# Kernel tuning notes

Hardware: AMD Instinct MI355X
Metric: run time of the kernel (lower is better)

Reference implementation:

```python
import jax, jax.numpy as jnp
import numpy as np

D_MODEL = 1024
D_INNER = 2048
D_STATE = 16
D_CONV = 4
DT_RANK = 128  # ceil(d_inner/16)
B, L = 4, 2048


def setup_inputs() -> dict:
    key = jax.random.key(0)
    ks = jax.random.split(key, 12)
    s = 0.02
    return {
        "x": jax.random.normal(ks[0], (B, L, D_MODEL), jnp.float32),
        "in_proj_w": jax.random.normal(ks[1], (2 * D_INNER, D_MODEL), jnp.float32) * s,
        "in_proj_b": jax.random.normal(ks[2], (2 * D_INNER,), jnp.float32) * s,
        "conv_w": jax.random.normal(ks[3], (D_INNER, 1, D_CONV), jnp.float32) * s,
        "conv_b": jax.random.normal(ks[4], (D_INNER,), jnp.float32) * s,
        "x_proj_w": jax.random.normal(ks[5], (DT_RANK + 2 * D_STATE, D_INNER), jnp.float32) * s,
        "dt_proj_w": jax.random.normal(ks[6], (D_INNER, DT_RANK), jnp.float32) * s,
        "dt_proj_b": jax.random.normal(ks[7], (D_INNER,), jnp.float32) * s,
        "A_log": jnp.log(jnp.tile(jnp.arange(1, D_STATE + 1, dtype=jnp.float32)[None, :], (D_INNER, 1))),
        "D": jnp.ones((D_INNER,), jnp.float32),
        "out_proj_w": jax.random.normal(ks[8], (D_MODEL, D_INNER), jnp.float32) * s,
        "out_proj_b": jax.random.normal(ks[9], (D_MODEL,), jnp.float32) * s,
    }


def _selective_scan(u, delta, A, B_ssm, C, Dp):
    # u, delta: [b, l, d]; B_ssm, C: [b, l, n]; A: [d, n]; Dp: [d]
    def step(h, inp):
        dlt, Bt, Ct, ut = inp  # [b,d],[b,n],[b,n],[b,d]
        dA = jnp.exp(dlt[..., None] * A)               # [b,d,n]
        dBu = dlt[..., None] * Bt[:, None, :] * ut[..., None]
        h = dA * h + dBu
        y = jnp.einsum('bdn,bn->bd', h, Ct)
        return h, y

    h0 = jnp.zeros((u.shape[0], A.shape[0], A.shape[1]), u.dtype)
    xs = (jnp.swapaxes(delta, 0, 1), jnp.swapaxes(B_ssm, 0, 1),
          jnp.swapaxes(C, 0, 1), jnp.swapaxes(u, 0, 1))
    _, ys = jax.lax.scan(step, h0, xs)                 # [l,b,d]
    return jnp.swapaxes(ys, 0, 1) + u * Dp             # [b,l,d]


def reference(x, in_proj_w, in_proj_b, conv_w, conv_b, x_proj_w,
              dt_proj_w, dt_proj_b, A_log, D, out_proj_w, out_proj_b):
    xr = x @ in_proj_w.T + in_proj_b                   # [b,l,2d]
    xc, res = jnp.split(xr, 2, axis=-1)
    # depthwise conv1d, torch padding='same' with k=4 -> pad (1, 2)
    xcl = jnp.swapaxes(xc, 1, 2)                       # [b,d,l]
    xcl = jax.lax.conv_general_dilated(
        xcl, conv_w, window_strides=(1,), padding=[(1, 2)],
        feature_group_count=D_INNER,
        dimension_numbers=('NCH', 'OIH', 'NCH')) + conv_b[None, :, None]
    xc = jnp.swapaxes(xcl, 1, 2)                       # [b,l,d]
    x_dbl = xc @ x_proj_w.T                            # [b,l,dt_rank+2n]
    d_dt, B_ssm, C = jnp.split(x_dbl, [DT_RANK, DT_RANK + D_STATE], axis=-1)
    delta = jax.nn.softplus(d_dt @ dt_proj_w.T + dt_proj_b)
    A = -jnp.exp(A_log)
    y = _selective_scan(xc, delta, A, B_ssm, C, D)     # [b,l,d]
    y = y * jax.nn.silu(res)
    return y @ out_proj_w.T + out_proj_b
```

## Files before the change

kernel.cpp:

```cpp
#include <hip/hip_runtime.h>
#include <hip/hip_bf16.h>
#include <hip/hip_fp16.h>


typedef _Float16 f16;
typedef __attribute__((ext_vector_type(4))) float f32x4;
typedef __attribute__((ext_vector_type(4))) _Float16 f16x4;
typedef __attribute__((ext_vector_type(8))) _Float16 f16x8;

#define AS1C(p) ((const __attribute__((address_space(1))) void*)(p))
#define AS3(p)  ((__attribute__((address_space(3))) void*)(p))

#define D_MODEL 1024
#define D_INNER 2048
#define LSEQ    2048
#define NB      4
#define NCH     32
#define CLEN    64
#define LOG2E   1.44269504f

__global__ void cvt_f32_to_f16(const float* __restrict__ in, f16* __restrict__ out, int n4) {
  int i = blockIdx.x * blockDim.x + threadIdx.x;
  if (i >= n4) return;
  f32x4 v = *(const f32x4*)(in + (size_t)i * 4);
  f16x4 o;
  o[0] = (f16)v[0]; o[1] = (f16)v[1]; o[2] = (f16)v[2]; o[3] = (f16)v[3];
  *(f16x4*)(out + (size_t)i * 4) = o;
}

__global__ void cvt_pad_xproj(const float* __restrict__ in, f16* __restrict__ out) {
  int i = blockIdx.x * blockDim.x + threadIdx.x;
  int idx = i << 2;
  int row = idx >> 11;
  f16x4 o;
  if (row < 160) {
    f32x4 v = *(const f32x4*)(in + idx);
    o[0] = (f16)v[0]; o[1] = (f16)v[1]; o[2] = (f16)v[2]; o[3] = (f16)v[3];
  } else {
    o[0] = (f16)0.f; o[1] = (f16)0.f; o[2] = (f16)0.f; o[3] = (f16)0.f;
  }
  *(f16x4*)(out + idx) = o;
}

template<int EPI, bool XSW>
__global__ __launch_bounds__(256) void gemm_f16(
    const f16* __restrict__ A, int lda,
    const f16* __restrict__ Bw, int K,
    const float* __restrict__ bias,
    void* __restrict__ O0, void* __restrict__ O1,
    int NV, int ldo, int gx)
{
  __shared__ f16 lA[128 * 32];
  __shared__ f16 lB[128 * 32];
  const int tid  = threadIdx.x;
  const int lane = tid & 63;
  const int wid  = tid >> 6;
  const int wr = wid >> 1, wc = wid & 1;

  int tn_i, tm_i;
  {
    const int bid = blockIdx.x;
    if constexpr (XSW) {
      const int nxs = gx >> 3;
      const int xcd = bid & 7;
      const int j   = bid >> 3;
      tn_i = xcd * nxs + j % nxs;
      tm_i = j / nxs;
    } else {
      tn_i = bid % gx;
      tm_i = bid / gx;
    }
  }
  const int tm = tm_i * 128, tn = tn_i * 128;

  f32x4 acc[4][4] = {};

  const int i4 = lane >> 2;
  const int k8 = (lane & 3) << 3;
  const int ca = wid << 1;
  const f16* Abase = A  + (size_t)(tm + ca * 16 + i4) * lda + k8;
  const f16* Bbase = Bw + (size_t)(tn + ca * 16 + i4) * K   + k8;

  const int nKT = K >> 5;
  for (int kt = 0; kt < nKT; ++kt) {
    const int ko = kt << 5;
    __syncthreads();
    __builtin_amdgcn_global_load_lds(AS1C(Abase + ko),                    AS3(lA + ca * 512),       16, 0, 0);
    __builtin_amdgcn_global_load_lds(AS1C(Abase + (size_t)16 * lda + ko), AS3(lA + ca * 512 + 512), 16, 0, 0);
    __builtin_amdgcn_global_load_lds(AS1C(Bbase + ko),                    AS3(lB + ca * 512),       16, 0, 0);
    __builtin_amdgcn_global_load_lds(AS1C(Bbase + (size_t)16 * K + ko),   AS3(lB + ca * 512 + 512), 16, 0, 0);
    __syncthreads();

    const int ro = lane & 15;
    const int kf = (lane >> 4) << 3;
    f16x8 af[4], bf[4];
#pragma unroll
    for (int mi = 0; mi < 4; ++mi)
      af[mi] = *(const f16x8*)(lA + (wr * 64 + mi * 16 + ro) * 32 + kf);
#pragma unroll
    for (int nj = 0; nj < 4; ++nj)
      bf[nj] = *(const f16x8*)(lB + (wc * 64 + nj * 16 + ro) * 32 + kf);
#pragma unroll
    for (int mi = 0; mi < 4; ++mi)
#pragma unroll
      for (int nj = 0; nj < 4; ++nj)
        acc[mi][nj] = __builtin_amdgcn_mfma_f32_16x16x32_f16(af[mi], bf[nj], acc[mi][nj], 0, 0, 0);
  }

#pragma unroll
  for (int mi = 0; mi < 4; ++mi) {
    const int rb = tm + wr * 64 + mi * 16 + ((lane >> 4) << 2);
#pragma unroll
    for (int nj = 0; nj < 4; ++nj) {
      const int gn = tn + wc * 64 + nj * 16 + (lane & 15);
      if (gn >= NV) continue;
      float bv = 0.f;
      if constexpr (EPI != 1) bv = bias[gn];
#pragma unroll
      for (int j = 0; j < 4; ++j) {
        const float v = acc[mi][nj][j] + bv;
        const size_t row = (size_t)(rb + j);
        if constexpr (EPI == 0) {
          if (gn < 2048) ((f16*)O0)[row * 2048 + gn] = (f16)v;
          else           ((f16*)O1)[row * 2048 + (gn - 2048)] = (f16)v;
        } else if constexpr (EPI == 1) {
          ((f16*)O0)[row * (size_t)ldo + gn] = (f16)v;
        } else if constexpr (EPI == 2) {
          const float sp = (v > 20.f) ? v : log1pf(__expf(v));
          ((f16*)O0)[row * (size_t)ldo + gn] = (f16)sp;
        } else {
          ((float*)O0)[row * (size_t)ldo + gn] = v;
        }
      }
    }
  }
}

__global__ __launch_bounds__(256) void conv1d_kernel(
    const f16* __restrict__ xin, const float* __restrict__ w,
    const float* __restrict__ cb, f16* __restrict__ xout)
{
  const int d0  = threadIdx.x << 3;
  const int bid = blockIdx.x;
  const int b   = bid >> 8;
  const int l0  = (bid & 255) << 3;
  float wv[4][8];
#pragma unroll
  for (int q = 0; q < 8; ++q) {
    f32x4 t = *(const f32x4*)(w + (size_t)(d0 + q) * 4);
    wv[0][q] = t[0]; wv[1][q] = t[1]; wv[2][q] = t[2]; wv[3][q] = t[3];
  }
  float bv[8];
  *(f32x4*)bv       = *(const f32x4*)(cb + d0);
  *(f32x4*)(bv + 4) = *(const f32x4*)(cb + d0 + 4);
  const size_t base = (size_t)b * LSEQ * D_INNER;
  for (int lt = l0; lt < l0 + 8; ++lt) {
    float acc[8];
#pragma unroll
    for (int q = 0; q < 8; ++q) acc[q] = bv[q];
#pragma unroll
    for (int j = 0; j < 4; ++j) {
      const int li = lt + j - 1;
      if (li < 0 || li >= LSEQ) continue;
      f16x8 v = *(const f16x8*)(xin + base + (size_t)li * D_INNER + d0);
#pragma unroll
      for (int q = 0; q < 8; ++q) acc[q] += wv[j][q] * (float)v[q];
    }
    f16x8 o;
#pragma unroll
    for (int q = 0; q < 8; ++q) o[q] = (f16)acc[q];
    *(f16x8*)(xout + base + (size_t)lt * D_INNER + d0) = o;
  }
}


__global__ __launch_bounds__(256) void scan_pass1(
    const f16* __restrict__ delta, const f16* __restrict__ u,
    const f16* __restrict__ xdbl, const float* __restrict__ A_log,
    float* __restrict__ chunkS, float* __restrict__ chunkH)
{
  const int tid = threadIdx.x;
  const int d = blockIdx.x * 256 + tid;
  const int c = blockIdx.y;
  const int b = blockIdx.z;
  __shared__ float bl[CLEN][16];
  {
    const int t = tid >> 2, q = tid & 3;
    if (q < 2) {
      f16x8 v = *(const f16x8*)(xdbl + ((size_t)(b * LSEQ + c * CLEN + t)) * 160 + 128 + q * 8);
      float* dst = &bl[t][q * 8];
#pragma unroll
      for (int e = 0; e < 8; ++e) dst[e] = (float)v[e];
    }
  }
  __syncthreads();

  float An2[16], h[16];
  const float* alp = A_log + (size_t)d * 16;
#pragma unroll
  for (int n = 0; n < 16; ++n) { An2[n] = -__expf(alp[n]) * LOG2E; h[n] = 0.f; }

  float dsum = 0.f;
  const size_t base = ((size_t)(b * LSEQ + c * CLEN)) * D_INNER + d;
  float dl[4], uu[4];
#pragma unroll
  for (int j = 0; j < 4; ++j) {
    dl[j] = (float)delta[base + (size_t)j * D_INNER];
    uu[j] = (float)u[base + (size_t)j * D_INNER];
  }
  for (int g = 0; g < CLEN / 4; ++g) {
    float ndl[4] = {0.f, 0.f, 0.f, 0.f}, nuu[4] = {0.f, 0.f, 0.f, 0.f};
    if (g < CLEN / 4 - 1) {
      const size_t nb = base + (size_t)(g + 1) * 4 * D_INNER;
#pragma unroll
      for (int j = 0; j < 4; ++j) {
        ndl[j] = (float)delta[nb + (size_t)j * D_INNER];
        nuu[j] = (float)u[nb + (size_t)j * D_INNER];
      }
    }
#pragma unroll
    for (int j = 0; j < 4; ++j) {
      const int t = g * 4 + j;
      const float du = dl[j] * uu[j];
      dsum += dl[j];
#pragma unroll
      for (int n = 0; n < 16; ++n) {
        const float dA = __builtin_amdgcn_exp2f(An2[n] * dl[j]);
        h[n] = dA * h[n] + du * bl[t][n];
      }
    }
#pragma unroll
    for (int j = 0; j < 4; ++j) { dl[j] = ndl[j]; uu[j] = nuu[j]; }
  }
  const size_t sb = ((size_t)b * NCH + c) * D_INNER + d;
  chunkS[sb] = dsum;
  const size_t ob = sb * 16;
#pragma unroll
  for (int q = 0; q < 4; ++q) {
    f32x4 vh;
#pragma unroll
    for (int j = 0; j < 4; ++j) vh[j] = h[q * 4 + j];
    *(f32x4*)(chunkH + ob + q * 4) = vh;
  }
}

__global__ __launch_bounds__(256) void scan_combine(
    const float* __restrict__ chunkS, const float* __restrict__ A_log,
    float* __restrict__ chunkH)
{
  const int i = blockIdx.x * 256 + threadIdx.x;
  const int b = i >> 15;
  const int dn = i & 32767;
  const int d = dn >> 4;
  const float An2 = -__expf(A_log[dn]) * LOG2E;
  const size_t hstride = (size_t)D_INNER * 16;
  size_t sIdx = (size_t)b * NCH * D_INNER + d;
  size_t hIdx = ((size_t)b * NCH * D_INNER) * 16 + dn;
  float hin = 0.f;
  for (int c = 0; c < NCH; ++c) {
    const float P  = __builtin_amdgcn_exp2f(An2 * chunkS[sIdx]);
    const float he = chunkH[hIdx];
    chunkH[hIdx] = hin;
    hin = P * hin + he;
    sIdx += D_INNER; hIdx += hstride;
  }
}

__global__ __launch_bounds__(256) void scan_pass2(
    const f16* __restrict__ delta, const f16* __restrict__ u,
    const f16* __restrict__ xdbl, const f16* __restrict__ res,
    const float* __restrict__ A_log, const float* __restrict__ Dp,
    const float* __restrict__ chunkH, f16* __restrict__ yg)
{
  const int tid = threadIdx.x;
  const int d = blockIdx.x * 256 + tid;
  const int c = blockIdx.y;
  const int b = blockIdx.z;
  __shared__ float bl[CLEN][16];
  __shared__ float cl[CLEN][16];
  {
    const int t = tid >> 2, q = tid & 3;
    f16x8 v = *(const f16x8*)(xdbl + ((size_t)(b * LSEQ + c * CLEN + t)) * 160 + 128 + q * 8);
    float* dst = (q < 2) ? &bl[t][(q & 1) * 8] : &cl[t][(q & 1) * 8];
#pragma unroll
    for (int e = 0; e < 8; ++e) dst[e] = (float)v[e];
  }
  __syncthreads();

  float An2[16], h[16];
  const float* alp = A_log + (size_t)d * 16;
#pragma unroll
  for (int n = 0; n < 16; ++n) An2[n] = -__expf(alp[n]) * LOG2E;
  const size_t hb = (((size_t)b * NCH + c) * D_INNER + d) * 16;
#pragma unroll
  for (int q = 0; q < 4; ++q) {
    f32x4 v = *(const f32x4*)(chunkH + hb + q * 4);
#pragma unroll
    for (int j = 0; j < 4; ++j) h[q * 4 + j] = v[j];
  }
  const float Dd = Dp[d];

  const size_t base = ((size_t)(b * LSEQ + c * CLEN)) * D_INNER + d;
  float dl[4], uu[4], rr[4];
#pragma unroll
  for (int j = 0; j < 4; ++j) {
    dl[j] = (float)delta[base + (size_t)j * D_INNER];
    uu[j] = (float)u[base + (size_t)j * D_INNER];
    rr[j] = (float)res[base + (size_t)j * D_INNER];
  }
  for (int g = 0; g < CLEN / 4; ++g) {
    float ndl[4] = {0.f, 0.f, 0.f, 0.f}, nuu[4] = {0.f, 0.f, 0.f, 0.f},
          nrr[4] = {0.f, 0.f, 0.f, 0.f};
    if (g < CLEN / 4 - 1) {
      const size_t nb = base + (size_t)(g + 1) * 4 * D_INNER;
#pragma unroll
      for (int j = 0; j < 4; ++j) {
        ndl[j] = (float)delta[nb + (size_t)j * D_INNER];
        nuu[j] = (float)u[nb + (size_t)j * D_INNER];
        nrr[j] = (float)res[nb + (size_t)j * D_INNER];
      }
    }
#pragma unroll
    for (int j = 0; j < 4; ++j) {
      const int t = g * 4 + j;
      const float du = dl[j] * uu[j];
      float y0 = 0.f, y1 = 0.f, y2 = 0.f, y3 = 0.f;
#pragma unroll
      for (int q = 0; q < 4; ++q) {
        float yp = 0.f;
#pragma unroll
        for (int e = 0; e < 4; ++e) {
          const int n = q * 4 + e;
          const float dA = __builtin_amdgcn_exp2f(An2[n] * dl[j]);
          h[n] = dA * h[n] + du * bl[t][n];
          yp += h[n] * cl[t][n];
        }
        if (q == 0) y0 = yp; else if (q == 1) y1 = yp; else if (q == 2) y2 = yp; else y3 = yp;
      }
      const float y = (y0 + y1) + (y2 + y3) + uu[j] * Dd;
      const float sil = rr[j] / (1.f + __expf(-rr[j]));
      yg[base + (size_t)t * D_INNER] = (f16)(y * sil);
    }
#pragma unroll
    for (int j = 0; j < 4; ++j) { dl[j] = ndl[j]; uu[j] = nuu[j]; rr[j] = nrr[j]; }
  }
}

extern "C" void kernel_launch(void* const* d_in, const int* in_sizes, int n_in,
                              void* d_out, int out_size, void* d_ws, size_t ws_size,
                              hipStream_t stream) {
  const float* x      = (const float*)d_in[0];
  const float* w_in_f = (const float*)d_in[1];
  const float* b_in   = (const float*)d_in[2];
  const float* conv_w = (const float*)d_in[3];
  const float* conv_b = (const float*)d_in[4];
  const float* w_xp_f = (const float*)d_in[5];
  const float* w_dt_f = (const float*)d_in[6];
  const float* b_dt   = (const float*)d_in[7];
  const float* A_log  = (const float*)d_in[8];
  const float* Dp     = (const float*)d_in[9];
  const float* w_ot_f = (const float*)d_in[10];
  const float* b_ot   = (const float*)d_in[11];

  char* ws = (char*)d_ws;
  size_t o = 0;
  auto alloc = [&](size_t bytes) -> char* {
    char* p = ws + o; o += (bytes + 255) & ~(size_t)255; return p;
  };
  f16* xf    = (f16*)alloc(16777216);
  f16* w_in  = (f16*)alloc(8388608);
  f16* w_xp  = (f16*)alloc(1048576);
  f16* w_dt  = (f16*)alloc(524288);
  f16* w_ot  = (f16*)alloc(4194304);
  f16* xcr   = (f16*)alloc(33554432);
  f16* res   = (f16*)alloc(33554432);
  f16* xc    = (f16*)alloc(33554432);
  f16* xdbl  = (f16*)alloc(2621440);
  f16* delta = (f16*)alloc(33554432);

  float* chunkH = (float*)xf;
  float* chunkS = (float*)w_in;

  dim3 blk(256);
  cvt_f32_to_f16<<<8192, blk, 0, stream>>>(x,      xf,   2097152);
  cvt_f32_to_f16<<<4096, blk, 0, stream>>>(w_in_f, w_in, 1048576);
  cvt_pad_xproj <<<512,  blk, 0, stream>>>(w_xp_f, w_xp);
  cvt_f32_to_f16<<<256,  blk, 0, stream>>>(w_dt_f, w_dt, 65536);
  cvt_f32_to_f16<<<2048, blk, 0, stream>>>(w_ot_f, w_ot, 524288);

  gemm_f16<0, true><<<2048, blk, 0, stream>>>(xf, 1024, w_in, 1024, b_in,
                                              xcr, res, 4096, 2048, 32);
  conv1d_kernel<<<1024, blk, 0, stream>>>(xcr, conv_w, conv_b, xc);
  gemm_f16<1, false><<<128, blk, 0, stream>>>(xc, 2048, w_xp, 2048, nullptr,
                                              xdbl, nullptr, 160, 160, 2);
  gemm_f16<2, false><<<1024, blk, 0, stream>>>(xdbl, 160, w_dt, 128, b_dt,
                                               delta, nullptr, 2048, 2048, 16);
  scan_pass1  <<<dim3(8, NCH, NB), blk, 0, stream>>>(delta, xc, xdbl, A_log,
                                                     chunkS, chunkH);
  scan_combine<<<512, blk, 0, stream>>>(chunkS, A_log, chunkH);
  scan_pass2  <<<dim3(8, NCH, NB), blk, 0, stream>>>(delta, xc, xdbl, res,
                                                     A_log, Dp, chunkH, xcr);
  gemm_f16<3, true><<<512, blk, 0, stream>>>(xcr, 2048, w_ot, 2048, b_ot,
                                             d_out, nullptr, 1024, 1024, 8);
}
```

Baseline: 419.6 us.

## Add pipelined 256x256 in_proj GEMM and deepen scan prefetch to eight steps

Replaces the in_proj GEMM with a new 512-thread kernel that uses 256x256 tiles, 128 KB of double-buffered LDS with XOR swizzling, staggered global-to-LDS staging interleaved with MFMA phases, and s_setprio. The goal is more data reuse per tile and overlap of memory loads with matrix math. Separately, both scan passes now prefetch 8 timesteps instead of 4 to hide more global-load latency. Risks include higher register pressure, occupancy limited to one block per CU by the LDS use, and subtle correctness issues in the manual vmcnt waits.

```diff
diff --git a/kernel.cpp b/kernel.cpp
--- a/kernel.cpp
+++ b/kernel.cpp
@@ -40,6 +40,137 @@
     o[0] = (f16)0.f; o[1] = (f16)0.f; o[2] = (f16)0.f; o[3] = (f16)0.f;
   }
   *(f16x4*)(out + idx) = o;
+}
+
+__global__ __launch_bounds__(512) void gemm8p_in(
+    const f16* __restrict__ Aq, const f16* __restrict__ Bq,
+    const float* __restrict__ bias, f16* __restrict__ O0,
+    f16* __restrict__ O1, int K, int gxn)
+{
+  extern __shared__ char smem[];
+  const int tid  = threadIdx.x;
+  const int lane = tid & 63;
+  const int wid  = tid >> 6;
+  const int wm = wid >> 2, wn = wid & 3;
+
+  int tn_i, tm_i;
+  {
+    const int bid = blockIdx.x;
+    const int nxs = gxn >> 3;
+    const int xcd = bid & 7;
+    const int j   = bid >> 3;
+    tn_i = xcd * nxs + j % nxs;
+    tm_i = j / nxs;
+  }
+  const int tm = tm_i * 256, tn = tn_i * 256;
+
+  const size_t Kb = (size_t)K * 2;
+  const int s0 = tid, s1 = 512 + tid;
+  const int r0 = s0 >> 3, r1 = s1 >> 3;
+  const size_t sOff0 = (size_t)r0 * Kb + (size_t)(((s0 & 7) ^ (r0 & 7)) << 4);
+  const size_t sOff1 = (size_t)r1 * Kb + (size_t)(((s1 & 7) ^ (r1 & 7)) << 4);
+  const char* Ab = (const char*)Aq;
+  const char* Bb = (const char*)Bq;
+  const int woff = wid << 10;
+
+#define STAGE_A(buf, h, kt) do { \
+    const char* _s = Ab + (size_t)(tm + (h) * 128) * Kb + (size_t)(kt) * 128; \
+    char* _d = smem + (buf) * 65536 + (h) * 16384 + woff; \
+    __builtin_amdgcn_global_load_lds(AS1C(_s + sOff0), AS3(_d), 16, 0, 0); \
+    __builtin_amdgcn_global_load_lds(AS1C(_s + sOff1), AS3(_d + 8192), 16, 0, 0); \
+  } while (0)
+#define STAGE_B(buf, h, kt) do { \
+    const char* _s = Bb + (size_t)(tn + (h) * 128) * Kb + (size_t)(kt) * 128; \
+    char* _d = smem + (buf) * 65536 + 32768 + (h) * 16384 + woff; \
+    __builtin_amdgcn_global_load_lds(AS1C(_s + sOff0), AS3(_d), 16, 0, 0); \
+    __builtin_amdgcn_global_load_lds(AS1C(_s + sOff1), AS3(_d + 8192), 16, 0, 0); \
+  } while (0)
+
+  const int lr = lane & 15, kg = lane >> 4;
+#define LDA(buf, mi, ks) \
+    (*(const f16x8*)(smem + (buf) * 65536 + wm * 16384 + ((mi) * 16 + lr) * 128 \
+                     + ((((ks) * 4 + kg) ^ (((mi) * 16 + lr) & 7)) << 4)))
+#define LDB(buf, nj, ks) \
+    (*(const f16x8*)(smem + (buf) * 65536 + 32768 \
+                     + (((wn * 64 + (nj) * 16 + lr) >> 7) * 16384) \
+                     + ((wn * 64 + (nj) * 16 + lr) & 127) * 128 \
+                     + ((((ks) * 4 + kg) ^ ((wn * 64 + (nj) * 16 + lr) & 7)) << 4)))
+
+  f32x4 acc[8][4] = {};
+  f16x8 bf[4][2];
+  const int nKT = K >> 6;
+
+  STAGE_B(0, 0, 0); STAGE_B(0, 1, 0);
+  STAGE_A(0, 0, 0); STAGE_A(0, 1, 0);
+  STAGE_B(1, 0, 1); STAGE_B(1, 1, 1);
+
+  for (int t = 0; t < nKT; ++t) {
+    const int buf = t & 1;
+    if (t + 1 < nKT) STAGE_A((t + 1) & 1, 0, t + 1);
+    if (t == nKT - 1) asm volatile("s_waitcnt vmcnt(0)" ::: "memory");
+    else              asm volatile("s_waitcnt vmcnt(6)" ::: "memory");
+    __builtin_amdgcn_s_barrier();
+    __builtin_amdgcn_sched_barrier(0);
+    {
+#pragma unroll
+      for (int nj = 0; nj < 4; ++nj) {
+        bf[nj][0] = LDB(buf, nj, 0);
+        bf[nj][1] = LDB(buf, nj, 1);
+      }
+      f16x8 a00 = LDA(buf, 0, 0), a01 = LDA(buf, 0, 1);
+      f16x8 a10 = LDA(buf, 1, 0), a11 = LDA(buf, 1, 1);
+      __builtin_amdgcn_s_setprio(1);
+#pragma unroll
+      for (int nj = 0; nj < 4; ++nj) {
+        acc[0][nj] = __builtin_amdgcn_mfma_f32_16x16x32_f16(a00, bf[nj][0], acc[0][nj], 0, 0, 0);
+        acc[0][nj] = __builtin_amdgcn_mfma_f32_16x16x32_f16(a01, bf[nj][1], acc[0][nj], 0, 0, 0);
+        acc[1][nj] = __builtin_amdgcn_mfma_f32_16x16x32_f16(a10, bf[nj][0], acc[1][nj], 0, 0, 0);
+        acc[1][nj] = __builtin_amdgcn_mfma_f32_16x16x32_f16(a11, bf[nj][1], acc[1][nj], 0, 0, 0);
+      }
+      __builtin_amdgcn_s_setprio(0);
+    }
+    __builtin_amdgcn_s_barrier();
+#pragma unroll
+    for (int q = 1; q < 4; ++q) {
+      f16x8 a0k0 = LDA(buf, 2 * q, 0),     a0k1 = LDA(buf, 2 * q, 1);
+      f16x8 a1k0 = LDA(buf, 2 * q + 1, 0), a1k1 = LDA(buf, 2 * q + 1, 1);
+      if (q == 1)      { if (t + 1 < nKT) STAGE_A((t + 1) & 1, 1, t + 1); }
+      else if (q == 2) { if (t + 2 < nKT) STAGE_B(buf, 0, t + 2); }
+      else             { if (t + 2 < nKT) STAGE_B(buf, 1, t + 2); }
+      __builtin_amdgcn_s_barrier();
+      __builtin_amdgcn_s_setprio(1);
+#pragma unroll
+      for (int nj = 0; nj < 4; ++nj) {
+        acc[2 * q][nj]     = __builtin_amdgcn_mfma_f32_16x16x32_f16(a0k0, bf[nj][0], acc[2 * q][nj], 0, 0, 0);
+        acc[2 * q][nj]     = __builtin_amdgcn_mfma_f32_16x16x32_f16(a0k1, bf[nj][1], acc[2 * q][nj], 0, 0, 0);
+        acc[2 * q + 1][nj] = __builtin_amdgcn_mfma_f32_16x16x32_f16(a1k0, bf[nj][0], acc[2 * q + 1][nj], 0, 0, 0);
+        acc[2 * q + 1][nj] = __builtin_amdgcn_mfma_f32_16x16x32_f16(a1k1, bf[nj][1], acc[2 * q + 1][nj], 0, 0, 0);
+      }
+      __builtin_amdgcn_s_setprio(0);
+      __builtin_amdgcn_s_barrier();
+    }
+  }
+#undef STAGE_A
+#undef STAGE_B
+#undef LDA
+#undef LDB
+
+#pragma unroll
+  for (int mi = 0; mi < 8; ++mi) {
+    const int rb = tm + wm * 128 + mi * 16 + ((lane >> 4) << 2);
+#pragma unroll
+    for (int nj = 0; nj < 4; ++nj) {
+      const int gn = tn + wn * 64 + nj * 16 + (lane & 15);
+      const float bv = bias[gn];
+#pragma unroll
+      for (int j = 0; j < 4; ++j) {
+        const float v = acc[mi][nj][j] + bv;
+        const size_t row = (size_t)(rb + j);
+        if (gn < 2048) O0[row * 2048 + gn] = (f16)v;
+        else           O1[row * 2048 + (gn - 2048)] = (f16)v;
+      }
+    }
+  }
 }
 
 template<int EPI, bool XSW>
@@ -93,18 +224,18 @@
 
     const int ro = lane & 15;
     const int kf = (lane >> 4) << 3;
-    f16x8 af[4], bf[4];
+    f16x8 af[4], bfr[4];
 #pragma unroll
     for (int mi = 0; mi < 4; ++mi)
       af[mi] = *(const f16x8*)(lA + (wr * 64 + mi * 16 + ro) * 32 + kf);
 #pragma unroll
     for (int nj = 0; nj < 4; ++nj)
-      bf[nj] = *(const f16x8*)(lB + (wc * 64 + nj * 16 + ro) * 32 + kf);
+      bfr[nj] = *(const f16x8*)(lB + (wc * 64 + nj * 16 + ro) * 32 + kf);
 #pragma unroll
     for (int mi = 0; mi < 4; ++mi)
 #pragma unroll
       for (int nj = 0; nj < 4; ++nj)
-        acc[mi][nj] = __builtin_amdgcn_mfma_f32_16x16x32_f16(af[mi], bf[nj], acc[mi][nj], 0, 0, 0);
+        acc[mi][nj] = __builtin_amdgcn_mfma_f32_16x16x32_f16(af[mi], bfr[nj], acc[mi][nj], 0, 0, 0);
   }
 
 #pragma unroll
@@ -172,7 +303,6 @@
     *(f16x8*)(xout + base + (size_t)lt * D_INNER + d0) = o;
   }
 }
-
 
 __global__ __launch_bounds__(256) void scan_pass1(
     const f16* __restrict__ delta, const f16* __restrict__ u,
@@ -202,25 +332,25 @@
 
   float dsum = 0.f;
   const size_t base = ((size_t)(b * LSEQ + c * CLEN)) * D_INNER + d;
-  float dl[4], uu[4];
-#pragma unroll
-  for (int j = 0; j < 4; ++j) {
+  float dl[8], uu[8];
+#pragma unroll
+  for (int j = 0; j < 8; ++j) {
     dl[j] = (float)delta[base + (size_t)j * D_INNER];
     uu[j] = (float)u[base + (size_t)j * D_INNER];
   }
-  for (int g = 0; g < CLEN / 4; ++g) {
-    float ndl[4] = {0.f, 0.f, 0.f, 0.f}, nuu[4] = {0.f, 0.f, 0.f, 0.f};
-    if (g < CLEN / 4 - 1) {
-      const size_t nb = base + (size_t)(g + 1) * 4 * D_INNER;
-#pragma unroll
-      for (int j = 0; j < 4; ++j) {
+  for (int g = 0; g < CLEN / 8; ++g) {
+    float ndl[8] = {}, nuu[8] = {};
+    if (g < CLEN / 8 - 1) {
+      const size_t nb = base + (size_t)(g + 1) * 8 * D_INNER;
+#pragma unroll
+      for (int j = 0; j < 8; ++j) {
         ndl[j] = (float)delta[nb + (size_t)j * D_INNER];
         nuu[j] = (float)u[nb + (size_t)j * D_INNER];
       }
     }
 #pragma unroll
-    for (int j = 0; j < 4; ++j) {
-      const int t = g * 4 + j;
+    for (int j = 0; j < 8; ++j) {
+      const int t = g * 8 + j;
       const float du = dl[j] * uu[j];
       dsum += dl[j];
 #pragma unroll
@@ -230,7 +360,7 @@
       }
     }
 #pragma unroll
-    for (int j = 0; j < 4; ++j) { dl[j] = ndl[j]; uu[j] = nuu[j]; }
+    for (int j = 0; j < 8; ++j) { dl[j] = ndl[j]; uu[j] = nuu[j]; }
   }
   const size_t sb = ((size_t)b * NCH + c) * D_INNER + d;
   chunkS[sb] = dsum;
@@ -301,28 +431,27 @@
   const float Dd = Dp[d];
 
   const size_t base = ((size_t)(b * LSEQ + c * CLEN)) * D_INNER + d;
-  float dl[4], uu[4], rr[4];
-#pragma unroll
-  for (int j = 0; j < 4; ++j) {
+  float dl[8], uu[8], rr[8];
+#pragma unroll
+  for (int j = 0; j < 8; ++j) {
     dl[j] = (float)delta[base + (size_t)j * D_INNER];
     uu[j] = (float)u[base + (size_t)j * D_INNER];
     rr[j] = (float)res[base + (size_t)j * D_INNER];
   }
-  for (int g = 0; g < CLEN / 4; ++g) {
-    float ndl[4] = {0.f, 0.f, 0.f, 0.f}, nuu[4] = {0.f, 0.f, 0.f, 0.f},
-          nrr[4] = {0.f, 0.f, 0.f, 0.f};
-    if (g < CLEN / 4 - 1) {
-      const size_t nb = base + (size_t)(g + 1) * 4 * D_INNER;
-#pragma unroll
-      for (int j = 0; j < 4; ++j) {
+  for (int g = 0; g < CLEN / 8; ++g) {
+    float ndl[8] = {}, nuu[8] = {}, nrr[8] = {};
+    if (g < CLEN / 8 - 1) {
+      const size_t nb = base + (size_t)(g + 1) * 8 * D_INNER;
+#pragma unroll
+      for (int j = 0; j < 8; ++j) {
         ndl[j] = (float)delta[nb + (size_t)j * D_INNER];
         nuu[j] = (float)u[nb + (size_t)j * D_INNER];
         nrr[j] = (float)res[nb + (size_t)j * D_INNER];
       }
     }
 #pragma unroll
-    for (int j = 0; j < 4; ++j) {
-      const int t = g * 4 + j;
+    for (int j = 0; j < 8; ++j) {
+      const int t = g * 8 + j;
       const float du = dl[j] * uu[j];
       float y0 = 0.f, y1 = 0.f, y2 = 0.f, y3 = 0.f;
 #pragma unroll
@@ -342,7 +471,7 @@
       yg[base + (size_t)t * D_INNER] = (f16)(y * sil);
     }
 #pragma unroll
-    for (int j = 0; j < 4; ++j) { dl[j] = ndl[j]; uu[j] = nuu[j]; rr[j] = nrr[j]; }
+    for (int j = 0; j < 8; ++j) { dl[j] = ndl[j]; uu[j] = nuu[j]; rr[j] = nrr[j]; }
   }
 }
 
@@ -381,6 +510,9 @@
   float* chunkH = (float*)xf;
   float* chunkS = (float*)w_in;
 
+  (void)hipFuncSetAttribute((const void*)gemm8p_in,
+                            hipFuncAttributeMaxDynamicSharedMemorySize, 131072);
+
   dim3 blk(256);
   cvt_f32_to_f16<<<8192, blk, 0, stream>>>(x,      xf,   2097152);
   cvt_f32_to_f16<<<4096, blk, 0, stream>>>(w_in_f, w_in, 1048576);
@@ -388,8 +520,7 @@
   cvt_f32_to_f16<<<256,  blk, 0, stream>>>(w_dt_f, w_dt, 65536);
   cvt_f32_to_f16<<<2048, blk, 0, stream>>>(w_ot_f, w_ot, 524288);
 
-  gemm_f16<0, true><<<2048, blk, 0, stream>>>(xf, 1024, w_in, 1024, b_in,
-                                              xcr, res, 4096, 2048, 32);
+  gemm8p_in<<<512, 512, 131072, stream>>>(xf, w_in, b_in, xcr, res, 1024, 16);
   conv1d_kernel<<<1024, blk, 0, stream>>>(xcr, conv_w, conv_b, xc);
   gemm_f16<1, false><<<128, blk, 0, stream>>>(xc, 2048, w_xp, 2048, nullptr,
                                               xdbl, nullptr, 160, 160, 2);
```

Result: slower. 438.3 us (+4.5%).
